# Kernel optimization log

Measured on AMD Instinct MI355X. Metric: run time of the kernel, lower is better.

## Reference

```python
import jax, jax.numpy as jnp
import numpy as np


def _lstm_layer(x_sbi, w_ih, w_hh, b):
    """Custom LSTM layer with elu candidate/cell activations.
    x_sbi: [S, B, I]; w_ih: [4H, I]; w_hh: [4H, H]; b: [4H]. Gate order i,f,g,o.
    Returns outputs [S, B, H].
    """
    H = w_hh.shape[1]
    S, B, _ = x_sbi.shape
    # Precompute the input projection for all timesteps at once.
    xw = jnp.einsum('sbi,gi->sbg', x_sbi, w_ih) + b  # [S, B, 4H]

    def step(carry, xt):
        h, c = carry
        gates = xt + h @ w_hh.T  # [B, 4H]
        i = jax.nn.sigmoid(gates[:, 0 * H:1 * H])
        f = jax.nn.sigmoid(gates[:, 1 * H:2 * H])
        g = jax.nn.elu(gates[:, 2 * H:3 * H])      # custom cell activation
        o = jax.nn.sigmoid(gates[:, 3 * H:4 * H])
        c = f * c + i * g
        h = o * jax.nn.elu(c)                       # custom hidden activation
        return (h, c), h

    h0 = jnp.zeros((B, H), dtype=x_sbi.dtype)
    c0 = jnp.zeros((B, H), dtype=x_sbi.dtype)
    _, out = jax.lax.scan(step, (h0, c0), xw)
    return out  # [S, B, H]


def setup_inputs() -> dict:
    key = jax.random.key(0)
    ks = jax.random.split(key, 12)
    B, S, I, H = 256, 512, 64, 512
    s_in = 1.0 / np.sqrt(H)
    d = {
        'x': jax.random.normal(ks[0], (B, S, I), dtype=jnp.float32),
        'w_ih1': jax.random.normal(ks[1], (4 * H, I), dtype=jnp.float32) * s_in,
        'w_hh1': jax.random.normal(ks[2], (4 * H, H), dtype=jnp.float32) * s_in,
        'b1': jax.random.normal(ks[3], (4 * H,), dtype=jnp.float32) * s_in,
        'w_ih2': jax.random.normal(ks[4], (4 * H, H), dtype=jnp.float32) * s_in,
        'w_hh2': jax.random.normal(ks[5], (4 * H, H), dtype=jnp.float32) * s_in,
        'b2': jax.random.normal(ks[6], (4 * H,), dtype=jnp.float32) * s_in,
        'w_ih3': jax.random.normal(ks[7], (4 * H, H), dtype=jnp.float32) * s_in,
        'w_hh3': jax.random.normal(ks[8], (4 * H, H), dtype=jnp.float32) * s_in,
        'b3': jax.random.normal(ks[9], (4 * H,), dtype=jnp.float32) * s_in,
        'fc_w': jax.random.normal(ks[10], (1, H), dtype=jnp.float32) * s_in,
        'fc_b': jax.random.normal(ks[11], (1,), dtype=jnp.float32) * s_in,
    }
    return d


def reference(x, w_ih1, w_hh1, b1, w_ih2, w_hh2, b2, w_ih3, w_hh3, b3, fc_w, fc_b):
    # x: [B, S, I] -> seq-first [S, B, I] (matches torch permute(1,0,2))
    out = jnp.transpose(x, (1, 0, 2))
    out = _lstm_layer(out, w_ih1, w_hh1, b1)  # dropout = identity (eval)
    out = _lstm_layer(out, w_ih2, w_hh2, b2)
    out = _lstm_layer(out, w_ih3, w_hh3, b3)
    last = out[-1]                             # [B, H]
    return last @ fc_w.T + fc_b                # [B, 1]
```

## Files before the change

kernel.cpp:

```cpp
#include <hip/hip_runtime.h>
#include <stdint.h>
#include <stddef.h>

#define S_LEN 512
#define BATCH 256
#define NIN   64
#define HD    512
#define G4    2048

typedef _Float16 f16;
typedef _Float16 f16x8 __attribute__((ext_vector_type(8)));
typedef float    f32x4 __attribute__((ext_vector_type(4)));
typedef uint32_t u32x4 __attribute__((ext_vector_type(4)));

__global__ void k_f32_to_f16(const float* __restrict__ src, f16* __restrict__ dst, int n) {
  int i = blockIdx.x * 256 + threadIdx.x;
  if (i < n) dst[i] = (f16)src[i];
}

__global__ void k_x_transpose(const float* __restrict__ x, f16* __restrict__ xin) {
  int idx = blockIdx.x * 256 + threadIdx.x;
  int i  = idx & 63;
  int sb = idx >> 6;
  int b  = sb & 255;
  int s  = sb >> 8;
  xin[idx] = (f16)x[((size_t)b * S_LEN + s) * NIN + i];
}

__global__ void k_zero_i32(uint32_t* p, int n) {
  int i = blockIdx.x * 256 + threadIdx.x;
  if (i < n) p[i] = 0u;
}

template<int K>
__global__ __launch_bounds__(256) void k_proj(const f16* __restrict__ A,
                                              const f16* __restrict__ W,
                                              const float* __restrict__ bias,
                                              f16* __restrict__ C) {
  constexpr int PITCH = 40;
  __shared__ f16 lA[128 * PITCH];
  __shared__ f16 lB[128 * PITCH];
  const int m0 = blockIdx.x * 128;
  const int n0 = blockIdx.y * 128;
  const int tid  = threadIdx.x;
  const int lane = tid & 63;
  const int wave = tid >> 6;
  const int wm = (wave & 1) * 64;
  const int wn = (wave >> 1) * 64;
  const int ln = lane & 15;
  const int quad = lane >> 4;
  const int r  = tid >> 1;
  const int ce = (tid & 1) * 16;

  f32x4 acc[4][4] = {};

  for (int kb = 0; kb < K; kb += 32) {
    const f16* ga = A + (size_t)(m0 + r) * K + kb + ce;
    const f16* gb = W + (size_t)(n0 + r) * K + kb + ce;
    u32x4 a0 = *(const u32x4*)ga;
    u32x4 a1 = *(const u32x4*)(ga + 8);
    u32x4 b0 = *(const u32x4*)gb;
    u32x4 b1 = *(const u32x4*)(gb + 8);
    __syncthreads();
    *(u32x4*)&lA[r * PITCH + ce]     = a0;
    *(u32x4*)&lA[r * PITCH + ce + 8] = a1;
    *(u32x4*)&lB[r * PITCH + ce]     = b0;
    *(u32x4*)&lB[r * PITCH + ce + 8] = b1;
    __syncthreads();
    f16x8 af[4], bf[4];
#pragma unroll
    for (int i = 0; i < 4; i++) {
      af[i] = *(const f16x8*)&lA[(wm + i * 16 + ln) * PITCH + quad * 8];
      bf[i] = *(const f16x8*)&lB[(wn + i * 16 + ln) * PITCH + quad * 8];
    }
#pragma unroll
    for (int mi = 0; mi < 4; mi++)
#pragma unroll
      for (int ni = 0; ni < 4; ni++)
        acc[mi][ni] = __builtin_amdgcn_mfma_f32_16x16x32_f16(af[mi], bf[ni], acc[mi][ni], 0, 0, 0);
  }

#pragma unroll
  for (int ni = 0; ni < 4; ni++) {
    const int n = n0 + wn + ni * 16 + ln;
    const float bv = bias[n];
#pragma unroll
    for (int mi = 0; mi < 4; mi++) {
#pragma unroll
      for (int rr = 0; rr < 4; rr++) {
        const int m = m0 + wm + mi * 16 + quad * 4 + rr;
        C[(size_t)m * G4 + n] = (f16)(acc[mi][ni][rr] + bv);
      }
    }
  }
}

__global__ __launch_bounds__(512, 2) void k_recur(
    const f16* __restrict__ Whh,
    const f16* __restrict__ xw,
    f16* __restrict__ ring,
    int* __restrict__ flags,
    f16* __restrict__ hclean,
    float* __restrict__ cbuf,
    int t0, int T, int cleanAll) {
  const int tid  = threadIdx.x;
  const int lane = tid & 63;
  const int wave = tid >> 6;
  const int gi = blockIdx.x >> 4;
  const int bi = blockIdx.x & 15;
  const int ln = lane & 15;
  const int quad = lane >> 4;

  __shared__ f16  lh[16 * 520];
  __shared__ float lgate[16 * 132];

  const int grow = (wave >> 1) * HD + gi * 32 + (wave & 1) * 16 + ln;
  f16x8 wf[16];
#pragma unroll
  for (int ks = 0; ks < 16; ks++) {
    u32x4 t = *(const u32x4*)(Whh + (size_t)grow * HD + ks * 32 + quad * 8);
    asm volatile("" : "+v"(t));
    wf[ks] = __builtin_bit_cast(f16x8, t);
  }

  const int b_  = tid >> 5;
  const int hl_ = tid & 31;
  float cv = 0.f;
  if (t0 != 0) cv = cbuf[(size_t)(bi * 16 + b_) * HD + gi * 32 + hl_];

  const int* fl = flags + bi * 16;
  int* myflag = flags + bi * 16 + gi;
  uint64_t* lh64 = (uint64_t*)lh;

  for (int tt = 0; tt < T; tt++) {
    const int t = t0 + tt;

    const f16* xwp = xw + (size_t)(tt * 256 + bi * 16 + b_) * G4 + gi * 32 + hl_;
    float xg0 = (float)xwp[0];
    float xg1 = (float)xwp[512];
    float xg2 = (float)xwp[1024];
    float xg3 = (float)xwp[1536];

    {
      int v = __hip_atomic_load(fl + (lane & 15), __ATOMIC_RELAXED, __HIP_MEMORY_SCOPE_AGENT);
      while (!__all(v >= t)) {
        __builtin_amdgcn_s_sleep(1);
        v = __hip_atomic_load(fl + (lane & 15), __ATOMIC_RELAXED, __HIP_MEMORY_SCOPE_AGENT);
      }
    }
    asm volatile("" ::: "memory");

    const uint64_t* hin64 = (const uint64_t*)(ring + (size_t)(t & 3) * (BATCH * HD)
                                              + (size_t)(bi * 16) * HD);
    uint64_t d[4];
#pragma unroll
    for (int j = 0; j < 4; j++)
      d[j] = __hip_atomic_load(hin64 + j * 512 + tid, __ATOMIC_RELAXED, __HIP_MEMORY_SCOPE_AGENT);
#pragma unroll
    for (int j = 0; j < 4; j++) {
      const int e   = j * 512 + tid;
      const int row = e >> 7;
      const int c8  = e & 127;
      lh64[row * 130 + c8] = d[j];
    }
    __syncthreads();

    f32x4 acc = {0.f, 0.f, 0.f, 0.f};
#pragma unroll
    for (int ks = 0; ks < 16; ks++) {
      f16x8 af = *(const f16x8*)&lh[ln * 520 + ks * 32 + quad * 8];
      acc = __builtin_amdgcn_mfma_f32_16x16x32_f16(af, wf[ks], acc, 0, 0, 0);
    }
    const int gcol = (wave >> 1) * 32 + (wave & 1) * 16 + ln;
#pragma unroll
    for (int rr = 0; rr < 4; rr++)
      lgate[(quad * 4 + rr) * 132 + gcol] = acc[rr];
    __syncthreads();

    {
      float gi_ = lgate[b_ * 132 + 0  + hl_] + xg0;
      float gf_ = lgate[b_ * 132 + 32 + hl_] + xg1;
      float gg_ = lgate[b_ * 132 + 64 + hl_] + xg2;
      float go_ = lgate[b_ * 132 + 96 + hl_] + xg3;
      const float ig = 1.f / (1.f + expf(-gi_));
      const float fg = 1.f / (1.f + expf(-gf_));
      const float gg = gg_ > 0.f ? gg_ : expm1f(gg_);
      const float og = 1.f / (1.f + expf(-go_));
      cv = fg * cv + ig * gg;
      const float hv = og * (cv > 0.f ? cv : expm1f(cv));
      f16 hv16 = (f16)hv;
      unsigned short us;
      __builtin_memcpy(&us, &hv16, 2);
      const size_t col = (size_t)(bi * 16 + b_) * HD + gi * 32 + hl_;
      __hip_atomic_store((unsigned short*)(ring + (size_t)((t + 1) & 3) * (BATCH * HD) + col),
                         us, __ATOMIC_RELAXED, __HIP_MEMORY_SCOPE_AGENT);
      if (cleanAll)
        hclean[(size_t)(tt * 256 + bi * 16 + b_) * HD + gi * 32 + hl_] = hv16;
      else if (tt == T - 1)
        hclean[(size_t)(bi * 16 + b_) * HD + gi * 32 + hl_] = hv16;
    }
    __syncthreads();
    if (tid == 0)
      __hip_atomic_store(myflag, t + 1, __ATOMIC_RELAXED, __HIP_MEMORY_SCOPE_AGENT);
  }

  cbuf[(size_t)(bi * 16 + b_) * HD + gi * 32 + hl_] = cv;
}

__global__ __launch_bounds__(64) void k_fc(const f16* __restrict__ hlast,
                                           const float* __restrict__ fcw,
                                           const float* __restrict__ fcb,
                                           float* __restrict__ out) {
  const int b = blockIdx.x, lane = threadIdx.x;
  const f16* hp = hlast + (size_t)b * HD + lane * 8;
  float s = 0.f;
#pragma unroll
  for (int j = 0; j < 8; j++) s += (float)hp[j] * fcw[lane * 8 + j];
  for (int off = 32; off; off >>= 1) s += __shfl_down(s, off);
  if (lane == 0) out[b] = s + fcb[0];
}

extern "C" void kernel_launch(void* const* d_in, const int* in_sizes, int n_in,
                              void* d_out, int out_size, void* d_ws, size_t ws_size,
                              hipStream_t stream) {
  (void)in_sizes; (void)n_in; (void)out_size;
  const float* x      = (const float*)d_in[0];
  const float* wih[3] = {(const float*)d_in[1], (const float*)d_in[4], (const float*)d_in[7]};
  const float* whh[3] = {(const float*)d_in[2], (const float*)d_in[5], (const float*)d_in[8]};
  const float* bia[3] = {(const float*)d_in[3], (const float*)d_in[6], (const float*)d_in[9]};
  const float* fcw = (const float*)d_in[10];
  const float* fcb = (const float*)d_in[11];
  float* out = (float*)d_out;

  char* ws = (char*)d_ws;
  size_t off = 0;
  auto alloc = [&](size_t bytes) -> char* {
    off = (off + 255) & ~(size_t)255;
    char* p = ws + off;
    off += bytes;
    return p;
  };

  f16* xin = (f16*)alloc((size_t)S_LEN * BATCH * NIN * 2);
  f16* wih16[3];
  wih16[0] = (f16*)alloc((size_t)G4 * NIN * 2);
  wih16[1] = (f16*)alloc((size_t)G4 * HD * 2);
  wih16[2] = (f16*)alloc((size_t)G4 * HD * 2);
  f16* whh16[3];
  for (int l = 0; l < 3; l++) whh16[l] = (f16*)alloc((size_t)G4 * HD * 2);
  float* cbuf[3];
  for (int l = 0; l < 3; l++) cbuf[l] = (float*)alloc((size_t)BATCH * HD * 4);
  f16* ring[3];
  for (int l = 0; l < 3; l++) ring[l] = (f16*)alloc((size_t)4 * BATCH * HD * 2);
  int* flags = (int*)alloc(3 * 256 * 4);
  f16* hclean2 = (f16*)alloc((size_t)BATCH * HD * 2);

  int T = 64;
  while (T > 4) {
    size_t need = off + 8 * 256
                + 2 * ((size_t)T * BATCH * HD * 2 + 256)
                + (size_t)T * BATCH * G4 * 2;
    if (need <= ws_size) break;
    T >>= 1;
  }
  f16* hclean01[2];
  hclean01[0] = (f16*)alloc((size_t)T * BATCH * HD * 2);
  hclean01[1] = (f16*)alloc((size_t)T * BATCH * HD * 2);
  f16* xw = (f16*)alloc((size_t)T * BATCH * G4 * 2);

  {
    int n = S_LEN * BATCH * NIN;
    k_x_transpose<<<dim3(n / 256), dim3(256), 0, stream>>>(x, xin);
  }
  k_f32_to_f16<<<dim3((G4 * NIN + 255) / 256), dim3(256), 0, stream>>>(wih[0], wih16[0], G4 * NIN);
  k_f32_to_f16<<<dim3((G4 * HD + 255) / 256), dim3(256), 0, stream>>>(wih[1], wih16[1], G4 * HD);
  k_f32_to_f16<<<dim3((G4 * HD + 255) / 256), dim3(256), 0, stream>>>(wih[2], wih16[2], G4 * HD);
  for (int l = 0; l < 3; l++)
    k_f32_to_f16<<<dim3((G4 * HD + 255) / 256), dim3(256), 0, stream>>>(whh[l], whh16[l], G4 * HD);
  for (int l = 0; l < 3; l++)
    k_zero_i32<<<dim3(BATCH * HD / 2 / 256), dim3(256), 0, stream>>>((uint32_t*)ring[l],
                                                                     BATCH * HD / 2);
  k_zero_i32<<<dim3(3), dim3(256), 0, stream>>>((uint32_t*)flags, 3 * 256);

  for (int t0 = 0; t0 < S_LEN; t0 += T) {
    for (int l = 0; l < 3; l++) {
      dim3 pg(T * BATCH / 128, G4 / 128);
      if (l == 0) {
        const f16* Achunk = xin + (size_t)t0 * BATCH * NIN;
        k_proj<NIN><<<pg, dim3(256), 0, stream>>>(Achunk, wih16[0], bia[0], xw);
      } else {
        k_proj<HD><<<pg, dim3(256), 0, stream>>>(hclean01[l - 1], wih16[l], bia[l], xw);
      }
      f16* hc = (l == 2) ? hclean2 : hclean01[l];
      k_recur<<<dim3(256), dim3(512), 0, stream>>>(whh16[l], xw, ring[l], flags + l * 256,
                                                   hc, cbuf[l], t0, T, l != 2);
    }
  }

  k_fc<<<dim3(BATCH), dim3(64), 0, stream>>>(hclean2, fcw, fcb, out);
}
```

Before: 5.465 ms.

## Use XCC-local cached ring loads/stores when a batch group shares one XCC

Each recurrent block reads its XCC ID from a hardware register and publishes it in a shared buffer tagged with an epoch. Blocks then check whether every block in their batch group sits on the same XCC. When they do, the hidden-state ring is exchanged with plain stores and sc0 loads that stay in the XCC's L2, instead of device-scope atomics. This is meant to cut per-timestep latency on the serial recurrence. It adds a startup handshake per launch and depends on the hardware's block-to-XCC placement and coherence behaviour being correct.

```diff
diff --git a/kernel.cpp b/kernel.cpp
--- a/kernel.cpp
+++ b/kernel.cpp
@@ -100,9 +100,10 @@
     const f16* __restrict__ xw,
     f16* __restrict__ ring,
     int* __restrict__ flags,
+    int* __restrict__ xccbuf,
     f16* __restrict__ hclean,
     float* __restrict__ cbuf,
-    int t0, int T, int cleanAll) {
+    int t0, int T, int cleanAll, int epoch) {
   const int tid  = threadIdx.x;
   const int lane = tid & 63;
   const int wave = tid >> 6;
@@ -123,6 +124,29 @@
     wf[ks] = __builtin_bit_cast(f16x8, t);
   }
 
+  const uint32_t myxcc = __builtin_amdgcn_s_getreg((31u << 11) | 20u) & 0xffu;
+  if (tid == 0)
+    __hip_atomic_store(xccbuf + blockIdx.x, (epoch << 8) | (int)myxcc,
+                       __ATOMIC_RELAXED, __HIP_MEMORY_SCOPE_AGENT);
+  bool local;
+  {
+    int slot = (lane < 16) ? (lane * 16 + bi)
+             : (lane < 32) ? (gi * 16 + (lane - 16))
+             : (int)blockIdx.x;
+    const int* xp = xccbuf + slot;
+    int e = __hip_atomic_load(xp, __ATOMIC_RELAXED, __HIP_MEMORY_SCOPE_AGENT);
+    while (!__all((e >> 8) == epoch)) {
+      __builtin_amdgcn_s_sleep(1);
+      e = __hip_atomic_load(xp, __ATOMIC_RELAXED, __HIP_MEMORY_SCOPE_AGENT);
+    }
+    const int x = e & 0xff;
+    const int g0 = __shfl(x, 0);
+    const bool groupUni = __all(lane >= 16 || x == g0);
+    const int c0 = __shfl(x, 16);
+    const bool ctrlUni  = __all(lane < 16 || lane >= 32 || x == c0);
+    local = groupUni && !ctrlUni;
+  }
+
   const int b_  = tid >> 5;
   const int hl_ = tid & 31;
   float cv = 0.f;
@@ -153,9 +177,23 @@
     const uint64_t* hin64 = (const uint64_t*)(ring + (size_t)(t & 3) * (BATCH * HD)
                                               + (size_t)(bi * 16) * HD);
     uint64_t d[4];
-#pragma unroll
-    for (int j = 0; j < 4; j++)
-      d[j] = __hip_atomic_load(hin64 + j * 512 + tid, __ATOMIC_RELAXED, __HIP_MEMORY_SCOPE_AGENT);
+    if (local) {
+      const uint64_t* a0 = hin64 + tid;
+      asm volatile(
+          "global_load_dwordx2 %0, %4, off sc0\n\t"
+          "global_load_dwordx2 %1, %5, off sc0\n\t"
+          "global_load_dwordx2 %2, %6, off sc0\n\t"
+          "global_load_dwordx2 %3, %7, off sc0\n\t"
+          "s_waitcnt vmcnt(0)"
+          : "=&v"(d[0]), "=&v"(d[1]), "=&v"(d[2]), "=&v"(d[3])
+          : "v"(a0), "v"(a0 + 512), "v"(a0 + 1024), "v"(a0 + 1536)
+          : "memory");
+    } else {
+#pragma unroll
+      for (int j = 0; j < 4; j++)
+        d[j] = __hip_atomic_load(hin64 + j * 512 + tid, __ATOMIC_RELAXED,
+                                 __HIP_MEMORY_SCOPE_AGENT);
+    }
 #pragma unroll
     for (int j = 0; j < 4; j++) {
       const int e   = j * 512 + tid;
@@ -192,8 +230,9 @@
       unsigned short us;
       __builtin_memcpy(&us, &hv16, 2);
       const size_t col = (size_t)(bi * 16 + b_) * HD + gi * 32 + hl_;
-      __hip_atomic_store((unsigned short*)(ring + (size_t)((t + 1) & 3) * (BATCH * HD) + col),
-                         us, __ATOMIC_RELAXED, __HIP_MEMORY_SCOPE_AGENT);
+      unsigned short* rp = (unsigned short*)(ring + (size_t)((t + 1) & 3) * (BATCH * HD) + col);
+      if (local) *rp = us;
+      else __hip_atomic_store(rp, us, __ATOMIC_RELAXED, __HIP_MEMORY_SCOPE_AGENT);
       if (cleanAll)
         hclean[(size_t)(tt * 256 + bi * 16 + b_) * HD + gi * 32 + hl_] = hv16;
       else if (tt == T - 1)
@@ -253,6 +292,7 @@
   f16* ring[3];
   for (int l = 0; l < 3; l++) ring[l] = (f16*)alloc((size_t)4 * BATCH * HD * 2);
   int* flags = (int*)alloc(3 * 256 * 4);
+  int* xccbuf = (int*)alloc(256 * 4);
   f16* hclean2 = (f16*)alloc((size_t)BATCH * HD * 2);
 
   int T = 64;
@@ -280,9 +320,10 @@
   for (int l = 0; l < 3; l++)
     k_zero_i32<<<dim3(BATCH * HD / 2 / 256), dim3(256), 0, stream>>>((uint32_t*)ring[l],
                                                                      BATCH * HD / 2);
-  k_zero_i32<<<dim3(3), dim3(256), 0, stream>>>((uint32_t*)flags, 3 * 256);
-
-  for (int t0 = 0; t0 < S_LEN; t0 += T) {
+  k_zero_i32<<<dim3(4), dim3(256), 0, stream>>>((uint32_t*)flags, 3 * 256 + 256);
+
+  int chunkIdx = 0;
+  for (int t0 = 0; t0 < S_LEN; t0 += T, chunkIdx++) {
     for (int l = 0; l < 3; l++) {
       dim3 pg(T * BATCH / 128, G4 / 128);
       if (l == 0) {
@@ -292,8 +333,9 @@
         k_proj<HD><<<pg, dim3(256), 0, stream>>>(hclean01[l - 1], wih16[l], bia[l], xw);
       }
       f16* hc = (l == 2) ? hclean2 : hclean01[l];
+      const int epoch = 1 + chunkIdx * 3 + l;
       k_recur<<<dim3(256), dim3(512), 0, stream>>>(whh16[l], xw, ring[l], flags + l * 256,
-                                                   hc, cbuf[l], t0, T, l != 2);
+                                                   xccbuf, hc, cbuf[l], t0, T, l != 2, epoch);
     }
   }
 
```

Result: slower. 5.845 ms (+6.9%).
